# Kernel optimization log

Measured on AMD Instinct MI355X. Metric: run time of the kernel, lower is better.

Reference implementation:

```python
import jax, jax.numpy as jnp
import numpy as np

B, T, C, H, KV, D = 2, 2048, 1024, 16, 4, 64
VE_GATE_CH = 32


def _rope(x, cos, sin):
    # x: (B,T,h,D); cos/sin: (1,T,1,D//2); half-split rotary
    d = x.shape[-1] // 2
    x1, x2 = x[..., :d], x[..., d:]
    return jnp.concatenate([x1 * cos + x2 * sin, -x1 * sin + x2 * cos], axis=-1)


def _rms_norm(x, eps=1.1920929e-07):
    # F.rms_norm with no weight; eps defaults to finfo(fp32).eps
    return x * jax.lax.rsqrt(jnp.mean(x * x, axis=-1, keepdims=True) + eps)


def setup_inputs() -> dict:
    key = jax.random.key(0)
    ks = jax.random.split(key, 8)
    x = jax.random.normal(ks[0], (B, T, C), dtype=jnp.float32)
    ve = jax.random.normal(ks[1], (B, T, KV * D), dtype=jnp.float32)
    # standard RoPE tables, half-dim = D//2
    inv_freq = 1.0 / (10000.0 ** (np.arange(0, D, 2, dtype=np.float32) / D))  # (32,)
    freqs = np.arange(T, dtype=np.float32)[:, None] * inv_freq[None, :]       # (T,32)
    cos = jnp.asarray(np.cos(freqs))[None, :, None, :]
    sin = jnp.asarray(np.sin(freqs))[None, :, None, :]
    s = 0.02
    Wq = jax.random.normal(ks[2], (C, H * D), dtype=jnp.float32) * s
    Wk = jax.random.normal(ks[3], (C, KV * D), dtype=jnp.float32) * s
    Wv = jax.random.normal(ks[4], (C, KV * D), dtype=jnp.float32) * s
    Wo = jax.random.normal(ks[5], (C, C), dtype=jnp.float32) * s
    Wg = jax.random.normal(ks[6], (VE_GATE_CH, KV), dtype=jnp.float32) * s
    return {"x": x, "ve": ve, "cos": cos, "sin": sin,
            "Wq": Wq, "Wk": Wk, "Wv": Wv, "Wo": Wo, "Wg": Wg,
            "window": 1024}


def reference(x, ve, cos, sin, Wq, Wk, Wv, Wo, Wg, window):
    b, t, c = x.shape
    q = (x @ Wq).reshape(b, t, H, D)
    k = (x @ Wk).reshape(b, t, KV, D)
    v = (x @ Wv).reshape(b, t, KV, D)
    # value-embedding gating: gate = 2*sigmoid(x[..., :32] @ Wg)
    gate = 2.0 * jax.nn.sigmoid(x[..., :VE_GATE_CH] @ Wg)  # (B,T,KV)
    v = v + gate[..., None] * ve.reshape(b, t, KV, D)
    q = _rms_norm(_rope(q, cos, sin))
    k = _rms_norm(_rope(k, cos, sin))
    # GQA: repeat_interleave kv heads to match query heads
    groups = H // KV
    k = jnp.repeat(k, groups, axis=2)  # (B,T,H,D)
    v = jnp.repeat(v, groups, axis=2)
    scale = 1.0 / jnp.sqrt(jnp.asarray(D, dtype=q.dtype))
    scores = jnp.einsum("bthd,bshd->bhts", q, k) * scale  # (B,H,T,T)
    rows = jnp.arange(t)[:, None]
    cols = jnp.arange(t)[None, :]
    mask = (cols <= rows) & (cols > rows - window)  # causal sliding window
    scores = jnp.where(mask[None, None], scores, jnp.finfo(scores.dtype).min)
    attn = jax.nn.softmax(scores, axis=-1)
    y = jnp.einsum("bhts,bshd->bthd", attn, v).reshape(b, t, c)
    return y @ Wo
```

## Files before the change

### kernel.cpp

```cpp
#include <hip/hip_runtime.h>
#include <hip/hip_bf16.h>

#define B_ 2
#define T_ 2048
#define C_ 1024
#define H_ 16
#define KV_ 4
#define D_ 64
#define M_ (B_*T_)

typedef __attribute__((ext_vector_type(4))) float f32x4;
typedef __attribute__((ext_vector_type(8))) short bf16x8;

__device__ __forceinline__ float exp2fast(float x) {
  return __builtin_amdgcn_exp2f(x);
}

__device__ __forceinline__ unsigned short f2bfu(float f) {
  unsigned u = __builtin_bit_cast(unsigned, f);
  u += 0x7FFFu + ((u >> 16) & 1u);
  return (unsigned short)(u >> 16);
}

__device__ __forceinline__ short f2bf(float f) {
  return (short)f2bfu(f);
}

__device__ __forceinline__ float bf2f(short s) {
  unsigned u = ((unsigned)(unsigned short)s) << 16;
  return __builtin_bit_cast(float, u);
}

__device__ __forceinline__ unsigned cvtpk(float a, float b) {
  unsigned r;
  asm("v_cvt_pk_bf16_f32 %0, %1, %2" : "=v"(r) : "v"(a), "v"(b));
  return r;
}

__device__ __forceinline__ void gld_lds16(const void* g, void* l) {
  __builtin_amdgcn_global_load_lds(
      (const __attribute__((address_space(1))) void*)g,
      (__attribute__((address_space(3))) void*)l, 16, 0, 0);
}

__global__ __launch_bounds__(256) void k_cast(const float* __restrict__ in,
                                              short* __restrict__ out, int n) {
  int i = (blockIdx.x * 256 + threadIdx.x) * 4;
  if (i + 3 < n) {
    float4 f = *(const float4*)(in + i);
    short4 s;
    s.x = f2bf(f.x); s.y = f2bf(f.y); s.z = f2bf(f.z); s.w = f2bf(f.w);
    *(short4*)(out + i) = s;
  }
}

__global__ __launch_bounds__(256) void k_transpose_all(const float* __restrict__ Wq,
                                                       const float* __restrict__ Wk,
                                                       const float* __restrict__ Wv,
                                                       const float* __restrict__ Wo,
                                                       short* __restrict__ wT,
                                                       short* __restrict__ woT) {
  __shared__ float tile[32][33];
  int bx = blockIdx.x;
  const float* in; short* out; int Ncol, cb;
  if (bx < 32)      { in = Wq; out = wT;                       Ncol = 1024; cb = bx; }
  else if (bx < 40) { in = Wk; out = wT + (size_t)1024 * 1024; Ncol = 256;  cb = bx - 32; }
  else if (bx < 48) { in = Wv; out = wT + (size_t)1280 * 1024; Ncol = 256;  cb = bx - 40; }
  else              { in = Wo; out = woT;                      Ncol = 1024; cb = bx - 48; }
  const int R = 1024;
  int c0 = cb * 32, r0 = blockIdx.y * 32;
  int tx = threadIdx.x, ty = threadIdx.y;
#pragma unroll
  for (int i = 0; i < 32; i += 8)
    tile[ty + i][tx] = in[(size_t)(r0 + ty + i) * Ncol + c0 + tx];
  __syncthreads();
#pragma unroll
  for (int i = 0; i < 32; i += 8)
    out[(size_t)(c0 + ty + i) * R + r0 + tx] = f2bf(tile[tx][ty + i]);
}

__global__ __launch_bounds__(256) void k_gemm64(const short* __restrict__ A,
                                                const short* __restrict__ Bt,
                                                float* __restrict__ C,
                                                int M, int N, int K) {
  __shared__ short sA[64 * 64];
  __shared__ short sB[128 * 64];
  const int tid = threadIdx.x;
  const int wid = tid >> 6, lane = tid & 63;
  const int g = lane >> 4, c = lane & 15;
  const int wm = wid >> 1, wn = wid & 1;
  const int m0 = blockIdx.y * 64, n0 = blockIdx.x * 128;
  const int strow = tid >> 3;
  const int scol  = ((tid & 7) ^ (strow & 7)) * 8;
  const int sw = c & 7;

  const short* Ag = A + (size_t)(m0 + strow) * K + scol;
  const short* Bg = Bt + (size_t)(n0 + strow) * K + scol;
  const int ldbase = wid * 512;

  f32x4 acc[2][4] = {};

  for (int k0 = 0; k0 < K; k0 += 64) {
#pragma unroll
    for (int i = 0; i < 2; ++i)
      gld_lds16(Ag + (size_t)(i * 32) * K + k0, &sA[i * 2048 + ldbase]);
#pragma unroll
    for (int i = 0; i < 4; ++i)
      gld_lds16(Bg + (size_t)(i * 32) * K + k0, &sB[i * 2048 + ldbase]);
    __syncthreads();
#pragma unroll
    for (int kk = 0; kk < 2; ++kk) {
      bf16x8 af[2], bfr[4];
#pragma unroll
      for (int i = 0; i < 2; ++i)
        af[i] = *(const bf16x8*)&sA[(wm * 32 + i * 16 + c) * 64 + ((kk * 4 + g) ^ sw) * 8];
#pragma unroll
      for (int j = 0; j < 4; ++j)
        bfr[j] = *(const bf16x8*)&sB[(wn * 64 + j * 16 + c) * 64 + ((kk * 4 + g) ^ sw) * 8];
#pragma unroll
      for (int i = 0; i < 2; ++i)
#pragma unroll
        for (int j = 0; j < 4; ++j)
          acc[i][j] = __builtin_amdgcn_mfma_f32_16x16x32_bf16(af[i], bfr[j], acc[i][j], 0, 0, 0);
    }
    __syncthreads();
  }
#pragma unroll
  for (int i = 0; i < 2; ++i)
#pragma unroll
    for (int j = 0; j < 4; ++j) {
      int row = m0 + wm * 32 + i * 16 + g * 4;
      int col = n0 + wn * 64 + j * 16 + c;
      float* cp = C + (size_t)row * N + col;
#pragma unroll
      for (int r = 0; r < 4; ++r) cp[(size_t)r * N] = acc[i][j][r];
    }
}

__global__ __launch_bounds__(256) void k_gemm_qkv(const short* __restrict__ A,
                                                  const short* __restrict__ Bt,
                                                  short* __restrict__ qkvb,
                                                  short* __restrict__ qb,
                                                  short* __restrict__ kbb,
                                                  const float* __restrict__ cosp,
                                                  const float* __restrict__ sinp) {
  __shared__ short sA[64 * 64];
  __shared__ short sB[128 * 64];
  const int N = 1536, K = 1024;
  const int tid = threadIdx.x;
  const int wid = tid >> 6, lane = tid & 63;
  const int g = lane >> 4, c = lane & 15;
  const int wm = wid >> 1, wn = wid & 1;
  const int m0 = blockIdx.y * 64, n0 = blockIdx.x * 128;
  const int strow = tid >> 3;
  const int scol  = ((tid & 7) ^ (strow & 7)) * 8;
  const int sw = c & 7;

  const short* Ag = A + (size_t)(m0 + strow) * K + scol;
  const short* Bg = Bt + (size_t)(n0 + strow) * K + scol;
  const int ldbase = wid * 512;

  f32x4 acc[2][4] = {};

  for (int k0 = 0; k0 < K; k0 += 64) {
#pragma unroll
    for (int i = 0; i < 2; ++i)
      gld_lds16(Ag + (size_t)(i * 32) * K + k0, &sA[i * 2048 + ldbase]);
#pragma unroll
    for (int i = 0; i < 4; ++i)
      gld_lds16(Bg + (size_t)(i * 32) * K + k0, &sB[i * 2048 + ldbase]);
    __syncthreads();
#pragma unroll
    for (int kk = 0; kk < 2; ++kk) {
      bf16x8 af[2], bfr[4];
#pragma unroll
      for (int i = 0; i < 2; ++i)
        af[i] = *(const bf16x8*)&sA[(wm * 32 + i * 16 + c) * 64 + ((kk * 4 + g) ^ sw) * 8];
#pragma unroll
      for (int j = 0; j < 4; ++j)
        bfr[j] = *(const bf16x8*)&sB[(wn * 64 + j * 16 + c) * 64 + ((kk * 4 + g) ^ sw) * 8];
#pragma unroll
      for (int i = 0; i < 2; ++i)
#pragma unroll
        for (int j = 0; j < 4; ++j)
          acc[i][j] = __builtin_amdgcn_mfma_f32_16x16x32_bf16(af[i], bfr[j], acc[i][j], 0, 0, 0);
    }
    __syncthreads();
  }

  const int head = blockIdx.x * 2 + wn;
  const int b = m0 >> 11;
  const int tbase = (m0 & (T_ - 1)) + wm * 32;
  if (head < 20) {
    short* outbase = (head < 16)
        ? qb  + ((size_t)(b * H_ + head) * T_) * D_
        : kbb + ((size_t)(b * KV_ + (head - 16)) * T_) * D_;
#pragma unroll
    for (int i = 0; i < 2; ++i)
#pragma unroll
      for (int r = 0; r < 4; ++r) {
        const int t = tbase + i * 16 + g * 4 + r;
        const float ca = cosp[t * 32 + c],      sa = sinp[t * 32 + c];
        const float cbv = cosp[t * 32 + 16 + c], sbv = sinp[t * 32 + 16 + c];
        const float f0 = acc[i][0][r], f1 = acc[i][1][r];
        const float f2 = acc[i][2][r], f3 = acc[i][3][r];
        const float r0 = f0 * ca + f2 * sa;
        const float r1 = f1 * cbv + f3 * sbv;
        const float r2 = f2 * ca - f0 * sa;
        const float r3 = f3 * cbv - f1 * sbv;
        float ss = (r0 * r0 + r1 * r1) + (r2 * r2 + r3 * r3);
        ss += __shfl_xor(ss, 1);
        ss += __shfl_xor(ss, 2);
        ss += __shfl_xor(ss, 4);
        ss += __shfl_xor(ss, 8);
        const float sc = rsqrtf(ss * (1.0f / 64.0f) + 1.1920929e-07f);
        unsigned w0 = cvtpk(r0 * sc, r1 * sc);
        unsigned w1 = cvtpk(r2 * sc, r3 * sc);
        unsigned long long w = ((unsigned long long)w1 << 32) | w0;
        *(unsigned long long*)(outbase + (size_t)t * D_ + c * 4) = w;
      }
  } else {
#pragma unroll
    for (int i = 0; i < 2; ++i)
#pragma unroll
      for (int j = 0; j < 4; ++j) {
        int row = m0 + wm * 32 + i * 16 + g * 4;
        int col = n0 + wn * 64 + j * 16 + c;
        short* cp = qkvb + (size_t)row * N + col;
#pragma unroll
        for (int r = 0; r < 4; ++r) cp[(size_t)r * N] = f2bf(acc[i][j][r]);
      }
  }
}

__global__ __launch_bounds__(256) void k_vtrans(const short* __restrict__ qkvb,
                                                const float* __restrict__ ve,
                                                const float* __restrict__ x,
                                                const float* __restrict__ Wg,
                                                short* __restrict__ vT) {
  const int t0 = blockIdx.x * 64;
  const int bk = blockIdx.y;
  const int b = bk >> 2, kv = bk & 3;
  const int tx = threadIdx.x;
  const int ty = threadIdx.y;
  __shared__ float tile[64][65];
  __shared__ float sgate[64];
  if (ty == 0) {
    const int row = b * T_ + t0 + tx;
    const float* xr = x + (size_t)row * C_;
    float a = 0.0f;
#pragma unroll 8
    for (int kk = 0; kk < 32; ++kk) a = fmaf(xr[kk], Wg[kk * KV_ + kv], a);
    sgate[tx] = 2.0f / (1.0f + __expf(-a));
  }
  __syncthreads();
#pragma unroll
  for (int i = 0; i < 16; ++i) {
    const int tr = ty + 4 * i;
    const int row = b * T_ + t0 + tr;
    float gt = sgate[tr];
    float v = bf2f(qkvb[(size_t)row * 1536 + 1280 + kv * 64 + tx]);
    v = fmaf(gt, ve[(size_t)row * (KV_ * D_) + kv * 64 + tx], v);
    tile[tr][tx] = v;
  }
  __syncthreads();
#pragma unroll
  for (int i = 0; i < 16; ++i) {
    const int d = ty + 4 * i;
    vT[((size_t)bk * 64 + d) * T_ + t0 + tx] = f2bf(tile[tx][d]);
  }
}

__global__ __launch_bounds__(512, 6) void k_attn(const short* __restrict__ qg,
                                                 const short* __restrict__ kg,
                                                 const short* __restrict__ vg,
                                                 short* __restrict__ yb,
                                                 const int* __restrict__ winp) {
  const int wsz = *winp;
  const int qt = blockIdx.x, bh = blockIdx.y;
  const int b = bh >> 4, h = bh & 15;
  const int kvh = h >> 2;
  const int tid = threadIdx.x;
  const int wid = tid >> 6, lane = tid & 63;
  const int g = lane >> 4, c = lane & 15;
  const int t0 = qt * 128 + wid * 16;

  __shared__ short sK[2][64 * 64];
  __shared__ short sV[2][64 * 64];
  __shared__ short spt_all[8][16][72];
  short (*spt)[72] = spt_all[wid];

  const short* qbase = qg + ((size_t)(b * H_ + h) * T_ + t0) * D_;
  const bf16x8 bq0 = *(const bf16x8*)(qbase + c * D_ + g * 8);
  const bf16x8 bq1 = *(const bf16x8*)(qbase + c * D_ + 32 + g * 8);
  const short* kbase = kg + (size_t)(b * KV_ + kvh) * T_ * D_;
  const short* vbase = vg + (size_t)(b * KV_ + kvh) * D_ * T_;

  const int srow0 = tid >> 3;
  const int sq    = ((tid & 7) ^ (srow0 & 7)) * 8;
  const int ldst0 = wid * 512;

  float m = -20000.0f, l = 0.0f;
  f32x4 o[4] = {};

  int lo = t0 - wsz + 1; if (lo < 0) lo = 0;
  const int kt_lo_w = lo >> 6;
  const int kt_hi_w = (t0 + 15) >> 6;
  int lou = qt * 128 - wsz + 1; if (lou < 0) lou = 0;
  const int kt_lo_u = lou >> 6;
  const int kt_hi_u = 2 * qt + 1;
  const int qgl = t0 + c;
  const float SC2 = 0.125f * 1.44269504088896340736f;

  {
    const short* ksrc = kbase + (size_t)(kt_lo_u * 64 + srow0) * D_ + sq;
    gld_lds16(ksrc, &sK[0][ldst0]);
    const short* vsrc = vbase + (size_t)srow0 * T_ + kt_lo_u * 64 + sq;
    gld_lds16(vsrc, &sV[0][ldst0]);
  }
  __syncthreads();

  int cb = 0;
  for (int kt = kt_lo_u; kt <= kt_hi_u; ++kt) {
    const int kc0 = kt * 64;
    if (kt < kt_hi_u) {
      const short* ksrc = kbase + (size_t)((kt + 1) * 64 + srow0) * D_ + sq;
      gld_lds16(ksrc, &sK[cb ^ 1][ldst0]);
      const short* vsrc = vbase + (size_t)srow0 * T_ + (kt + 1) * 64 + sq;
      gld_lds16(vsrc, &sV[cb ^ 1][ldst0]);
    }
    if (kt >= kt_lo_w && kt <= kt_hi_w) {
      f32x4 s[4] = {};
#pragma unroll
      for (int cj = 0; cj < 4; ++cj) {
        const int rbase = (cj * 16 + c) * 64;
        const int sw = (c & 7);
        bf16x8 k0 = *(const bf16x8*)&sK[cb][rbase + ((g ^ sw) * 8)];
        bf16x8 k1 = *(const bf16x8*)&sK[cb][rbase + (((4 + g) ^ sw) * 8)];
        s[cj] = __builtin_amdgcn_mfma_f32_16x16x32_bf16(k0, bq0, s[cj], 0, 0, 0);
        s[cj] = __builtin_amdgcn_mfma_f32_16x16x32_bf16(k1, bq1, s[cj], 0, 0, 0);
      }
      const bool edge = (kt >= kt_hi_w) || (kt <= kt_lo_w + 1);
      float tmax = -3.0e38f;
#pragma unroll
      for (int cj = 0; cj < 4; ++cj)
#pragma unroll
        for (int r = 0; r < 4; ++r) {
          float v = s[cj][r];
          if (edge) {
            int kv = kc0 + cj * 16 + 4 * g + r;
            v = (kv <= qgl && kv > qgl - wsz) ? v : -1.0e9f;
            s[cj][r] = v;
          }
          tmax = fmaxf(tmax, v);
        }
      tmax = fmaxf(tmax, __shfl_xor(tmax, 16));
      tmax = fmaxf(tmax, __shfl_xor(tmax, 32));
      const float tms = tmax * SC2;
      if (!__all(tms <= m + 8.0f)) {
        const float nm = fmaxf(m, tms);
        const float fr = exp2fast(m - nm);
        m = nm;
        l *= fr;
#pragma unroll
        for (int nd = 0; nd < 4; ++nd)
#pragma unroll
          for (int r = 0; r < 4; ++r) o[nd][r] *= fr;
      }
      const float negm = -m;
      float psum = 0.0f;
      unsigned pb[8];
#pragma unroll
      for (int cj = 0; cj < 4; ++cj) {
        float p0 = exp2fast(fmaf(s[cj][0], SC2, negm));
        float p1 = exp2fast(fmaf(s[cj][1], SC2, negm));
        float p2 = exp2fast(fmaf(s[cj][2], SC2, negm));
        float p3 = exp2fast(fmaf(s[cj][3], SC2, negm));
        psum += (p0 + p1) + (p2 + p3);
        pb[2 * cj]     = cvtpk(p0, p1);
        pb[2 * cj + 1] = cvtpk(p2, p3);
      }
      psum += __shfl_xor(psum, 16);
      psum += __shfl_xor(psum, 32);
      l += psum;
#pragma unroll
      for (int cj = 0; cj < 4; ++cj) {
        unsigned long long w = ((unsigned long long)pb[2 * cj + 1] << 32) | pb[2 * cj];
        *(unsigned long long*)&spt[c][cj * 16 + 4 * g] = w;
      }
      asm volatile("s_waitcnt lgkmcnt(0)" ::: "memory");
#pragma unroll
      for (int ks = 0; ks < 2; ++ks) {
        bf16x8 bp = *(const bf16x8*)&spt[c][ks * 32 + g * 8];
#pragma unroll
        for (int nd = 0; nd < 4; ++nd) {
          const int rbase = (nd * 16 + c) * 64;
          bf16x8 bv = *(const bf16x8*)&sV[cb][rbase + (((ks * 4 + g) ^ (c & 7)) * 8)];
          o[nd] = __builtin_amdgcn_mfma_f32_16x16x32_bf16(bv, bp, o[nd], 0, 0, 0);
        }
      }
    }
    __syncthreads();
    cb ^= 1;
  }
  const float inv = 1.0f / l;
#pragma unroll
  for (int nd = 0; nd < 4; ++nd) {
    unsigned d0 = cvtpk(o[nd][0] * inv, o[nd][1] * inv);
    unsigned d1 = cvtpk(o[nd][2] * inv, o[nd][3] * inv);
    unsigned long long w = ((unsigned long long)d1 << 32) | d0;
    *(unsigned long long*)(yb + ((size_t)b * T_ + t0 + c) * C_ + h * D_ + nd * 16 + 4 * g) = w;
  }
}

extern "C" void kernel_launch(void* const* d_in, const int* in_sizes, int n_in,
                              void* d_out, int out_size, void* d_ws, size_t ws_size,
                              hipStream_t stream) {
  const float* x    = (const float*)d_in[0];
  const float* ve   = (const float*)d_in[1];
  const float* cosp = (const float*)d_in[2];
  const float* sinp = (const float*)d_in[3];
  const float* Wq   = (const float*)d_in[4];
  const float* Wk   = (const float*)d_in[5];
  const float* Wv   = (const float*)d_in[6];
  const float* Wo   = (const float*)d_in[7];
  const float* Wg   = (const float*)d_in[8];
  const int*   winp = (const int*)d_in[9];
  float* out = (float*)d_out;
  char* ws = (char*)d_ws;

  const size_t MB = 1024 * 1024;
  short* xb    = (short*)(ws);
  short* wT    = (short*)(ws + 8  * MB);
  short* woT   = (short*)(ws + 11 * MB);
  short* qkvb  = (short*)(ws + 13 * MB);
  short* qb    = (short*)(ws + 25 * MB);
  short* kbuf  = (short*)(ws + 33 * MB);
  short* vT    = (short*)(ws + 35 * MB);
  short* yb    = (short*)(ws + 37 * MB);

  k_cast<<<4096, 256, 0, stream>>>(x, xb, M_ * C_);
  k_transpose_all<<<dim3(80, 32), dim3(32, 8), 0, stream>>>(Wq, Wk, Wv, Wo, wT, woT);

  k_gemm_qkv<<<dim3(12, 64), 256, 0, stream>>>(xb, wT, qkvb, qb, kbuf, cosp, sinp);
  k_vtrans<<<dim3(32, 8), dim3(64, 4), 0, stream>>>(qkvb, ve, x, Wg, vT);
  k_attn<<<dim3(16, 32), 512, 0, stream>>>(qb, kbuf, vT, yb, winp);
  k_gemm64<<<dim3(8, 64), 256, 0, stream>>>(yb, woT, out, M_, 1024, 1024);
}
```

Measured before the change: 95.54 us.

## Double-buffer GEMM LDS tiles and shrink attention LDS for higher occupancy

Both projection GEMMs now double-buffer their shared-memory A/B tiles and prefetch the next K tile before computing the current one, which removes one barrier per iteration and overlaps loads with MFMA work. The attention kernel drops the V double buffer, loads V synchronously within each iteration, and halves the P staging buffer by writing and consuming P in two halves. Together with deferring the row-sum shuffle to the end, this cuts LDS use so the launch bound can rise from 6 to 8 blocks. The trade-offs are an extra barrier per attention tile, V loads that are no longer hidden behind the previous tile, and doubled LDS in the GEMMs, which may lower their occupancy.

```diff
diff --git a/kernel.cpp b/kernel.cpp
--- a/kernel.cpp
+++ b/kernel.cpp
@@ -83,8 +83,8 @@
                                                 const short* __restrict__ Bt,
                                                 float* __restrict__ C,
                                                 int M, int N, int K) {
-  __shared__ short sA[64 * 64];
-  __shared__ short sB[128 * 64];
+  __shared__ short sA[2][64 * 64];
+  __shared__ short sB[2][128 * 64];
   const int tid = threadIdx.x;
   const int wid = tid >> 6, lane = tid & 63;
   const int g = lane >> 4, c = lane & 15;
@@ -100,23 +100,33 @@
 
   f32x4 acc[2][4] = {};
 
+#pragma unroll
+  for (int i = 0; i < 2; ++i)
+    gld_lds16(Ag + (size_t)(i * 32) * K, &sA[0][i * 2048 + ldbase]);
+#pragma unroll
+  for (int i = 0; i < 4; ++i)
+    gld_lds16(Bg + (size_t)(i * 32) * K, &sB[0][i * 2048 + ldbase]);
+  __syncthreads();
+
+  int buf = 0;
   for (int k0 = 0; k0 < K; k0 += 64) {
-#pragma unroll
-    for (int i = 0; i < 2; ++i)
-      gld_lds16(Ag + (size_t)(i * 32) * K + k0, &sA[i * 2048 + ldbase]);
-#pragma unroll
-    for (int i = 0; i < 4; ++i)
-      gld_lds16(Bg + (size_t)(i * 32) * K + k0, &sB[i * 2048 + ldbase]);
-    __syncthreads();
+    if (k0 + 64 < K) {
+#pragma unroll
+      for (int i = 0; i < 2; ++i)
+        gld_lds16(Ag + (size_t)(i * 32) * K + k0 + 64, &sA[buf ^ 1][i * 2048 + ldbase]);
+#pragma unroll
+      for (int i = 0; i < 4; ++i)
+        gld_lds16(Bg + (size_t)(i * 32) * K + k0 + 64, &sB[buf ^ 1][i * 2048 + ldbase]);
+    }
 #pragma unroll
     for (int kk = 0; kk < 2; ++kk) {
       bf16x8 af[2], bfr[4];
 #pragma unroll
       for (int i = 0; i < 2; ++i)
-        af[i] = *(const bf16x8*)&sA[(wm * 32 + i * 16 + c) * 64 + ((kk * 4 + g) ^ sw) * 8];
+        af[i] = *(const bf16x8*)&sA[buf][(wm * 32 + i * 16 + c) * 64 + ((kk * 4 + g) ^ sw) * 8];
 #pragma unroll
       for (int j = 0; j < 4; ++j)
-        bfr[j] = *(const bf16x8*)&sB[(wn * 64 + j * 16 + c) * 64 + ((kk * 4 + g) ^ sw) * 8];
+        bfr[j] = *(const bf16x8*)&sB[buf][(wn * 64 + j * 16 + c) * 64 + ((kk * 4 + g) ^ sw) * 8];
 #pragma unroll
       for (int i = 0; i < 2; ++i)
 #pragma unroll
@@ -124,6 +134,7 @@
           acc[i][j] = __builtin_amdgcn_mfma_f32_16x16x32_bf16(af[i], bfr[j], acc[i][j], 0, 0, 0);
     }
     __syncthreads();
+    buf ^= 1;
   }
 #pragma unroll
   for (int i = 0; i < 2; ++i)
@@ -144,8 +155,8 @@
                                                   short* __restrict__ kbb,
                                                   const float* __restrict__ cosp,
                                                   const float* __restrict__ sinp) {
-  __shared__ short sA[64 * 64];
-  __shared__ short sB[128 * 64];
+  __shared__ short sA[2][64 * 64];
+  __shared__ short sB[2][128 * 64];
   const int N = 1536, K = 1024;
   const int tid = threadIdx.x;
   const int wid = tid >> 6, lane = tid & 63;
@@ -162,23 +173,33 @@
 
   f32x4 acc[2][4] = {};
 
+#pragma unroll
+  for (int i = 0; i < 2; ++i)
+    gld_lds16(Ag + (size_t)(i * 32) * K, &sA[0][i * 2048 + ldbase]);
+#pragma unroll
+  for (int i = 0; i < 4; ++i)
+    gld_lds16(Bg + (size_t)(i * 32) * K, &sB[0][i * 2048 + ldbase]);
+  __syncthreads();
+
+  int buf = 0;
   for (int k0 = 0; k0 < K; k0 += 64) {
-#pragma unroll
-    for (int i = 0; i < 2; ++i)
-      gld_lds16(Ag + (size_t)(i * 32) * K + k0, &sA[i * 2048 + ldbase]);
-#pragma unroll
-    for (int i = 0; i < 4; ++i)
-      gld_lds16(Bg + (size_t)(i * 32) * K + k0, &sB[i * 2048 + ldbase]);
-    __syncthreads();
+    if (k0 + 64 < K) {
+#pragma unroll
+      for (int i = 0; i < 2; ++i)
+        gld_lds16(Ag + (size_t)(i * 32) * K + k0 + 64, &sA[buf ^ 1][i * 2048 + ldbase]);
+#pragma unroll
+      for (int i = 0; i < 4; ++i)
+        gld_lds16(Bg + (size_t)(i * 32) * K + k0 + 64, &sB[buf ^ 1][i * 2048 + ldbase]);
+    }
 #pragma unroll
     for (int kk = 0; kk < 2; ++kk) {
       bf16x8 af[2], bfr[4];
 #pragma unroll
       for (int i = 0; i < 2; ++i)
-        af[i] = *(const bf16x8*)&sA[(wm * 32 + i * 16 + c) * 64 + ((kk * 4 + g) ^ sw) * 8];
+        af[i] = *(const bf16x8*)&sA[buf][(wm * 32 + i * 16 + c) * 64 + ((kk * 4 + g) ^ sw) * 8];
 #pragma unroll
       for (int j = 0; j < 4; ++j)
-        bfr[j] = *(const bf16x8*)&sB[(wn * 64 + j * 16 + c) * 64 + ((kk * 4 + g) ^ sw) * 8];
+        bfr[j] = *(const bf16x8*)&sB[buf][(wn * 64 + j * 16 + c) * 64 + ((kk * 4 + g) ^ sw) * 8];
 #pragma unroll
       for (int i = 0; i < 2; ++i)
 #pragma unroll
@@ -186,6 +207,7 @@
           acc[i][j] = __builtin_amdgcn_mfma_f32_16x16x32_bf16(af[i], bfr[j], acc[i][j], 0, 0, 0);
     }
     __syncthreads();
+    buf ^= 1;
   }
 
   const int head = blockIdx.x * 2 + wn;
@@ -271,7 +293,7 @@
   }
 }
 
-__global__ __launch_bounds__(512, 6) void k_attn(const short* __restrict__ qg,
+__global__ __launch_bounds__(512, 8) void k_attn(const short* __restrict__ qg,
                                                  const short* __restrict__ kg,
                                                  const short* __restrict__ vg,
                                                  short* __restrict__ yb,
@@ -286,9 +308,9 @@
   const int t0 = qt * 128 + wid * 16;
 
   __shared__ short sK[2][64 * 64];
-  __shared__ short sV[2][64 * 64];
-  __shared__ short spt_all[8][16][72];
-  short (*spt)[72] = spt_all[wid];
+  __shared__ short sV[64 * 64];
+  __shared__ short spt_all[8][16][40];
+  short (*spt)[40] = spt_all[wid];
 
   const short* qbase = qg + ((size_t)(b * H_ + h) * T_ + t0) * D_;
   const bf16x8 bq0 = *(const bf16x8*)(qbase + c * D_ + g * 8);
@@ -315,21 +337,25 @@
   {
     const short* ksrc = kbase + (size_t)(kt_lo_u * 64 + srow0) * D_ + sq;
     gld_lds16(ksrc, &sK[0][ldst0]);
-    const short* vsrc = vbase + (size_t)srow0 * T_ + kt_lo_u * 64 + sq;
-    gld_lds16(vsrc, &sV[0][ldst0]);
   }
   __syncthreads();
 
   int cb = 0;
   for (int kt = kt_lo_u; kt <= kt_hi_u; ++kt) {
     const int kc0 = kt * 64;
+    {
+      const short* vsrc = vbase + (size_t)srow0 * T_ + kc0 + sq;
+      gld_lds16(vsrc, &sV[ldst0]);
+    }
     if (kt < kt_hi_u) {
       const short* ksrc = kbase + (size_t)((kt + 1) * 64 + srow0) * D_ + sq;
       gld_lds16(ksrc, &sK[cb ^ 1][ldst0]);
-      const short* vsrc = vbase + (size_t)srow0 * T_ + (kt + 1) * 64 + sq;
-      gld_lds16(vsrc, &sV[cb ^ 1][ldst0]);
-    }
-    if (kt >= kt_lo_w && kt <= kt_hi_w) {
+    }
+    const bool active = (kt >= kt_lo_w && kt <= kt_hi_w);
+    unsigned pb[8];
+    float fr = 1.0f;
+    bool doresc = false;
+    if (active) {
       f32x4 s[4] = {};
 #pragma unroll
       for (int cj = 0; cj < 4; ++cj) {
@@ -357,19 +383,15 @@
       tmax = fmaxf(tmax, __shfl_xor(tmax, 16));
       tmax = fmaxf(tmax, __shfl_xor(tmax, 32));
       const float tms = tmax * SC2;
-      if (!__all(tms <= m + 8.0f)) {
+      doresc = !__all(tms <= m + 8.0f);
+      if (doresc) {
         const float nm = fmaxf(m, tms);
-        const float fr = exp2fast(m - nm);
+        fr = exp2fast(m - nm);
         m = nm;
         l *= fr;
-#pragma unroll
-        for (int nd = 0; nd < 4; ++nd)
-#pragma unroll
-          for (int r = 0; r < 4; ++r) o[nd][r] *= fr;
       }
       const float negm = -m;
       float psum = 0.0f;
-      unsigned pb[8];
 #pragma unroll
       for (int cj = 0; cj < 4; ++cj) {
         float p0 = exp2fast(fmaf(s[cj][0], SC2, negm));
@@ -380,29 +402,51 @@
         pb[2 * cj]     = cvtpk(p0, p1);
         pb[2 * cj + 1] = cvtpk(p2, p3);
       }
-      psum += __shfl_xor(psum, 16);
-      psum += __shfl_xor(psum, 32);
       l += psum;
-#pragma unroll
-      for (int cj = 0; cj < 4; ++cj) {
-        unsigned long long w = ((unsigned long long)pb[2 * cj + 1] << 32) | pb[2 * cj];
-        *(unsigned long long*)&spt[c][cj * 16 + 4 * g] = w;
+    }
+    __syncthreads();
+    if (active) {
+      {
+        unsigned long long w0 = ((unsigned long long)pb[1] << 32) | pb[0];
+        unsigned long long w1 = ((unsigned long long)pb[3] << 32) | pb[2];
+        *(unsigned long long*)&spt[c][4 * g]      = w0;
+        *(unsigned long long*)&spt[c][16 + 4 * g] = w1;
+      }
+      if (doresc) {
+#pragma unroll
+        for (int nd = 0; nd < 4; ++nd)
+#pragma unroll
+          for (int r = 0; r < 4; ++r) o[nd][r] *= fr;
       }
       asm volatile("s_waitcnt lgkmcnt(0)" ::: "memory");
-#pragma unroll
-      for (int ks = 0; ks < 2; ++ks) {
-        bf16x8 bp = *(const bf16x8*)&spt[c][ks * 32 + g * 8];
-#pragma unroll
-        for (int nd = 0; nd < 4; ++nd) {
-          const int rbase = (nd * 16 + c) * 64;
-          bf16x8 bv = *(const bf16x8*)&sV[cb][rbase + (((ks * 4 + g) ^ (c & 7)) * 8)];
-          o[nd] = __builtin_amdgcn_mfma_f32_16x16x32_bf16(bv, bp, o[nd], 0, 0, 0);
-        }
+      bf16x8 bp0 = *(const bf16x8*)&spt[c][8 * g];
+#pragma unroll
+      for (int nd = 0; nd < 4; ++nd) {
+        const int rbase = (nd * 16 + c) * 64;
+        bf16x8 bv = *(const bf16x8*)&sV[rbase + ((g ^ (c & 7)) * 8)];
+        o[nd] = __builtin_amdgcn_mfma_f32_16x16x32_bf16(bv, bp0, o[nd], 0, 0, 0);
+      }
+      asm volatile("s_waitcnt lgkmcnt(0)" ::: "memory");
+      {
+        unsigned long long w0 = ((unsigned long long)pb[5] << 32) | pb[4];
+        unsigned long long w1 = ((unsigned long long)pb[7] << 32) | pb[6];
+        *(unsigned long long*)&spt[c][4 * g]      = w0;
+        *(unsigned long long*)&spt[c][16 + 4 * g] = w1;
+      }
+      asm volatile("s_waitcnt lgkmcnt(0)" ::: "memory");
+      bf16x8 bp1 = *(const bf16x8*)&spt[c][8 * g];
+#pragma unroll
+      for (int nd = 0; nd < 4; ++nd) {
+        const int rbase = (nd * 16 + c) * 64;
+        bf16x8 bv = *(const bf16x8*)&sV[rbase + (((4 + g) ^ (c & 7)) * 8)];
+        o[nd] = __builtin_amdgcn_mfma_f32_16x16x32_bf16(bv, bp1, o[nd], 0, 0, 0);
       }
     }
     __syncthreads();
     cb ^= 1;
   }
+  l += __shfl_xor(l, 16);
+  l += __shfl_xor(l, 32);
   const float inv = 1.0f / l;
 #pragma unroll
   for (int nd = 0; nd < 4; ++nd) {
```

New measurement: 107.1 us. 12.1% more time.
